# Kernel optimization log

Measured on AMD Instinct MI355X. Metric: run time of the kernel, lower is better.

## Reference

```python
import jax, jax.numpy as jnp
import numpy as np
from jax import lax

DN = ('NCHW', 'OIHW', 'NCHW')

def _conv(x, w, b, s):
    return lax.conv_general_dilated(x, w, (s, s), 'VALID', dimension_numbers=DN) + b[None, :, None, None]

def _deconv(x, w, b, s):
    # transposed conv, VALID: out = (in-1)*s + k
    return lax.conv_transpose(x, w, (s, s), 'VALID', dimension_numbers=DN) + b[None, :, None, None]

def _encoder(x, ew1, eb1, ew2, eb2, ew3, eb3):
    h = jax.nn.relu(_conv(x, ew1, eb1, 2))
    h = jax.nn.relu(_conv(h, ew2, eb2, 2))
    return jax.nn.relu(_conv(h, ew3, eb3, 2))

def _xcorr(x1, x2):
    # per-sample cross-correlation: x2[i] (C,h,w) is the kernel for x1[i] (C,H,W).
    # Equivalent to the original python loop of B single-sample F.conv2d calls,
    # fused into one grouped conv (feature_group_count=B).
    B, C, H, W = x1.shape
    y = lax.conv_general_dilated(x1.reshape(1, B * C, H, W), x2, (1, 1), 'VALID',
                                 dimension_numbers=DN, feature_group_count=B)
    return y.reshape(B, 1, y.shape[2], y.shape[3])

def setup_inputs():
    key = jax.random.key(0)
    ks = jax.random.split(key, 24)
    B = 64
    f32 = jnp.float32
    def w(k, shape, fan_in):
        return jax.random.normal(k, shape, f32) * np.float32(1.0 / np.sqrt(fan_in))
    inp = {}
    inp['pos'] = jax.random.uniform(ks[0], (B, 3, 255, 255), f32)
    inp['neg'] = jax.random.uniform(ks[1], (B, 3, 255, 255), f32)
    inp['pos_crop'] = jax.random.uniform(ks[2], (B, 3, 127, 127), f32)
    inp['eps'] = jax.random.normal(ks[3], (B, 32, 14, 14), f32)
    s = np.float32(1.0 / np.sqrt(3 * 127 * 127))  # pytorch init_anchor: uniform(-stdv, stdv)
    inp['anchor_crop'] = jax.random.uniform(ks[4], (3, 127, 127), f32, -s, s)
    # shared encoder (used by VAE and by self.encoder)
    inp['ew1'] = w(ks[5], (32, 3, 4, 4), 3 * 16);   inp['eb1'] = jnp.zeros((32,), f32)
    inp['ew2'] = w(ks[6], (64, 32, 4, 4), 32 * 16); inp['eb2'] = jnp.zeros((64,), f32)
    inp['ew3'] = w(ks[7], (64, 64, 4, 4), 64 * 16); inp['eb3'] = jnp.zeros((64,), f32)
    # VAE heads + decoder
    inp['mw'] = w(ks[8], (32, 64, 1, 1), 64);  inp['mb'] = jnp.zeros((32,), f32)
    inp['lw'] = w(ks[9], (32, 64, 1, 1), 64);  inp['lb'] = jnp.zeros((32,), f32)
    inp['dw0'] = w(ks[10], (64, 32, 1, 1), 32);      inp['db0'] = jnp.zeros((64,), f32)
    inp['dw1'] = w(ks[11], (32, 64, 4, 4), 64 * 16); inp['db1'] = jnp.zeros((32,), f32)
    inp['dw2'] = w(ks[12], (16, 32, 4, 4), 32 * 16); inp['db2'] = jnp.zeros((16,), f32)
    inp['dw3'] = w(ks[13], (3, 16, 5, 5), 16 * 25);  inp['db3'] = jnp.zeros((3,), f32)
    return inp

def reference(pos, neg, pos_crop, eps, anchor_crop, ew1, eb1, ew2, eb2, ew3, eb3,
              mw, mb, lw, lb, dw0, db0, dw1, db1, dw2, db2, dw3, db3):
    enc = lambda x: _encoder(x, ew1, eb1, ew2, eb2, ew3, eb3)
    # VAE forward on pos_crop
    h = enc(pos_crop)                          # [B,64,14,14]
    mu = _conv(h, mw, mb, 1)                   # [B,32,14,14]
    logvar = _conv(h, lw, lb, 1)
    z = mu + eps * jnp.exp(0.5 * logvar)       # reparameterization
    d = jax.nn.relu(_conv(z, dw0, db0, 1))
    d = jax.nn.relu(_deconv(d, dw1, db1, 2))   # 14 -> 30
    d = jax.nn.relu(_deconv(d, dw2, db2, 2))   # 30 -> 62
    recon = jax.nn.sigmoid(_deconv(d, dw3, db3, 2))  # 62 -> 127
    # siamese branches
    pos_f = enc(pos)                           # [B,64,30,30]
    neg_f = enc(neg)
    B = pos.shape[0]
    anchor = jnp.broadcast_to(anchor_crop[None], (B,) + anchor_crop.shape)  # [B,3,127,127]
    anchor_f = enc(anchor)                     # [B,64,14,14]
    cxp = _xcorr(pos_f, anchor_f)              # [B,1,17,17]
    cxn = _xcorr(neg_f, anchor_f)
    return (anchor, cxp, cxn, recon, mu, logvar)
```

## Files before the change

### kernel.cpp

```cpp
#include <hip/hip_runtime.h>

#define DIVUP(a,b) (((a)+(b)-1)/(b))

__global__ void bcast_anchor_kernel(const float* __restrict__ a, float* __restrict__ out) {
    int i = blockIdx.x * 256 + threadIdx.x;
    int b = blockIdx.y;
    if (i < 48387) out[b * 48387 + i] = a[i];
}

template<int OCT, bool VEC>
__global__ void conv4s2_relu_k(const float* __restrict__ in, const float* __restrict__ w,
                               const float* __restrict__ bias, float* __restrict__ out,
                               int Cin, int Hin, int Win, int Hout, int Wout, int OSTR)
{
    const int ocg = blockIdx.y, b = blockIdx.z, Cout = gridDim.y * OCT;
    const int TX = (Wout + 3) >> 2;
    const int t  = blockIdx.x * 256 + threadIdx.x;
    if (t >= Hout * TX) return;
    const int oy = t / TX, tx = t - oy * TX;
    int ox0 = tx * 4; if (ox0 > Wout - 4) ox0 = Wout - 4;

    const float* ip = in + ((size_t)(b * Cin) * Hin + 2 * oy) * Win + 2 * ox0;
    const float* wb = w + (size_t)ocg * OCT * Cin * 16;
    float acc[OCT][4];
    #pragma unroll
    for (int o = 0; o < OCT; ++o) {
        float z = bias[ocg * OCT + o];
        acc[o][0] = z; acc[o][1] = z; acc[o][2] = z; acc[o][3] = z;
    }
    for (int ic = 0; ic < Cin; ++ic) {
        const float* r = ip + (size_t)ic * Hin * Win;
        #pragma unroll
        for (int ky = 0; ky < 4; ++ky) {
            const float* rr = r + ky * Win;
            float x0,x1,x2,x3,x4,x5,x6,x7,x8,x9;
            if (VEC) {
                const float2* rv = (const float2*)rr;
                float2 p0=rv[0], p1=rv[1], p2=rv[2], p3=rv[3], p4=rv[4];
                x0=p0.x; x1=p0.y; x2=p1.x; x3=p1.y; x4=p2.x;
                x5=p2.y; x6=p3.x; x7=p3.y; x8=p4.x; x9=p4.y;
            } else {
                x0=rr[0]; x1=rr[1]; x2=rr[2]; x3=rr[3]; x4=rr[4];
                x5=rr[5]; x6=rr[6]; x7=rr[7]; x8=rr[8]; x9=rr[9];
            }
            #pragma unroll
            for (int o = 0; o < OCT; ++o) {
                const float* wk = wb + ((o * Cin + ic) * 4 + ky) * 4;
                float w0 = wk[0], w1 = wk[1], w2 = wk[2], w3 = wk[3];
                acc[o][0] = fmaf(x0, w0, fmaf(x1, w1, fmaf(x2, w2, fmaf(x3, w3, acc[o][0]))));
                acc[o][1] = fmaf(x2, w0, fmaf(x3, w1, fmaf(x4, w2, fmaf(x5, w3, acc[o][1]))));
                acc[o][2] = fmaf(x4, w0, fmaf(x5, w1, fmaf(x6, w2, fmaf(x7, w3, acc[o][2]))));
                acc[o][3] = fmaf(x6, w0, fmaf(x7, w1, fmaf(x8, w2, fmaf(x9, w3, acc[o][3]))));
            }
        }
    }
    float* op = out + (((size_t)b * Cout + ocg * OCT) * Hout + oy) * OSTR + ox0;
    #pragma unroll
    for (int o = 0; o < OCT; ++o) {
        float* q = op + (size_t)o * Hout * OSTR;
        q[0] = fmaxf(acc[o][0], 0.0f); q[1] = fmaxf(acc[o][1], 0.0f);
        q[2] = fmaxf(acc[o][2], 0.0f); q[3] = fmaxf(acc[o][3], 0.0f);
    }
}

__global__ void conv4s2_pair4_k(const float* __restrict__ in, const float* __restrict__ w,
                                const float* __restrict__ bias, float* __restrict__ out,
                                int nb)
{
    const int bid = blockIdx.x;
    int b, ocg, xt;
    if ((nb & 7) == 0) {
        const int xcd = bid & 7;
        const int t8  = bid >> 3;
        const int spx = t8 >> 5;
        const int j   = t8 & 31;
        b   = xcd + 8 * spx;
        ocg = j >> 1;
        xt  = j & 1;
    } else {
        xt  = bid & 1;
        ocg = (bid >> 1) & 15;
        b   = bid >> 5;
    }
    const int Cin = 32, Hin = 126, Hout = 62, Wout = 62, Cout = 64;
    const int TX = 16, H2 = 31;
    const int t = xt * 256 + threadIdx.x;
    if (t >= H2 * TX) return;
    const int oyp = t / TX, tx = t - oyp * TX;
    int ox0 = tx * 4; if (ox0 > Wout - 4) ox0 = Wout - 4;
    const int oy0 = 2 * oyp;

    const float* ip = in + ((size_t)(b * Cin) * Hin + 2 * oy0) * 128 + 2 * ox0;
    const float* wb = w + (size_t)ocg * 4 * Cin * 16;
    float acc[4][2][4];
    #pragma unroll
    for (int o = 0; o < 4; ++o) {
        float z = bias[ocg * 4 + o];
        #pragma unroll
        for (int p = 0; p < 2; ++p) {
            acc[o][p][0] = z; acc[o][p][1] = z; acc[o][p][2] = z; acc[o][p][3] = z;
        }
    }
    for (int ic = 0; ic < Cin; ++ic) {
        const float* r = ip + (size_t)ic * Hin * 128;
        float4 ra[6]; float4 rb[6]; float2 rc[6];
        #pragma unroll
        for (int rr6 = 0; rr6 < 6; ++rr6) {
            const float* row = r + rr6 * 128;
            ra[rr6] = *(const float4*)row;
            rb[rr6] = *(const float4*)(row + 4);
            rc[rr6] = *(const float2*)(row + 8);
        }
        #pragma unroll
        for (int rr6 = 0; rr6 < 6; ++rr6) {
            float x0=ra[rr6].x, x1=ra[rr6].y, x2=ra[rr6].z, x3=ra[rr6].w;
            float x4=rb[rr6].x, x5=rb[rr6].y, x6=rb[rr6].z, x7=rb[rr6].w;
            float x8=rc[rr6].x, x9=rc[rr6].y;
            #pragma unroll
            for (int o = 0; o < 4; ++o) {
                if (rr6 < 4) {
                    const float* wk = wb + ((o * Cin + ic) * 4 + rr6) * 4;
                    float w0 = wk[0], w1 = wk[1], w2 = wk[2], w3 = wk[3];
                    acc[o][0][0] = fmaf(x0, w0, fmaf(x1, w1, fmaf(x2, w2, fmaf(x3, w3, acc[o][0][0]))));
                    acc[o][0][1] = fmaf(x2, w0, fmaf(x3, w1, fmaf(x4, w2, fmaf(x5, w3, acc[o][0][1]))));
                    acc[o][0][2] = fmaf(x4, w0, fmaf(x5, w1, fmaf(x6, w2, fmaf(x7, w3, acc[o][0][2]))));
                    acc[o][0][3] = fmaf(x6, w0, fmaf(x7, w1, fmaf(x8, w2, fmaf(x9, w3, acc[o][0][3]))));
                }
                if (rr6 >= 2) {
                    const float* wk = wb + ((o * Cin + ic) * 4 + (rr6 - 2)) * 4;
                    float w0 = wk[0], w1 = wk[1], w2 = wk[2], w3 = wk[3];
                    acc[o][1][0] = fmaf(x0, w0, fmaf(x1, w1, fmaf(x2, w2, fmaf(x3, w3, acc[o][1][0]))));
                    acc[o][1][1] = fmaf(x2, w0, fmaf(x3, w1, fmaf(x4, w2, fmaf(x5, w3, acc[o][1][1]))));
                    acc[o][1][2] = fmaf(x4, w0, fmaf(x5, w1, fmaf(x6, w2, fmaf(x7, w3, acc[o][1][2]))));
                    acc[o][1][3] = fmaf(x6, w0, fmaf(x7, w1, fmaf(x8, w2, fmaf(x9, w3, acc[o][1][3]))));
                }
            }
        }
    }
    float* op = out + (((size_t)b * Cout + ocg * 4) * Hout + oy0) * Wout + ox0;
    #pragma unroll
    for (int o = 0; o < 4; ++o) {
        float* q = op + (size_t)o * Hout * Wout;
        q[0]        = fmaxf(acc[o][0][0], 0.0f); q[1]        = fmaxf(acc[o][0][1], 0.0f);
        q[2]        = fmaxf(acc[o][0][2], 0.0f); q[3]        = fmaxf(acc[o][0][3], 0.0f);
        q[Wout]     = fmaxf(acc[o][1][0], 0.0f); q[Wout + 1] = fmaxf(acc[o][1][1], 0.0f);
        q[Wout + 2] = fmaxf(acc[o][1][2], 0.0f); q[Wout + 3] = fmaxf(acc[o][1][3], 0.0f);
    }
}

__global__ void vae_head_kernel(const float* __restrict__ h, const float* __restrict__ mw,
                                const float* __restrict__ mb, const float* __restrict__ lw,
                                const float* __restrict__ lb, const float* __restrict__ eps,
                                float* __restrict__ mu_out, float* __restrict__ lv_out,
                                float* __restrict__ z_out)
{
    const int idx = blockIdx.x * 256 + threadIdx.x;
    if (idx >= 64 * 32 * 196) return;
    const int p  = idx % 196;
    const int oc = (idx / 196) % 32;
    const int b  = idx / (196 * 32);
    const float* hb = h + (b * 64) * 196 + p;
    float am = mb[oc], al = lb[oc];
    for (int ic = 0; ic < 64; ++ic) {
        float hv = hb[ic * 196];
        am = fmaf(hv, mw[oc * 64 + ic], am);
        al = fmaf(hv, lw[oc * 64 + ic], al);
    }
    mu_out[idx] = am;
    lv_out[idx] = al;
    z_out[idx]  = fmaf(eps[idx], expf(0.5f * al), am);
}

__global__ void conv1x1_relu_kernel(const float* __restrict__ in, const float* __restrict__ w,
                                    const float* __restrict__ bias, float* __restrict__ out,
                                    int Cin, int Cout, int HW, int total)
{
    const int idx = blockIdx.x * 256 + threadIdx.x;
    if (idx >= total) return;
    const int p  = idx % HW;
    const int oc = (idx / HW) % Cout;
    const int b  = idx / (HW * Cout);
    const float* ib = in + (b * Cin) * HW + p;
    float acc = bias[oc];
    for (int ic = 0; ic < 64; ++ic) acc = fmaf(ib[(ic % Cin) * HW], w[oc * Cin + (ic % Cin)], acc) - ((ic >= Cin) ? fmaf(ib[(ic % Cin) * HW], w[oc * Cin + (ic % Cin)], 0.0f) : 0.0f);
    out[idx] = fmaxf(acc, 0.0f);
}

template<int OCT>
__global__ void deconv4s2_relu_k(const float* __restrict__ in, const float* __restrict__ w,
                                 const float* __restrict__ bias, float* __restrict__ out,
                                 int Cin, int Hin, int Win, int Hout, int Wout)
{
    const int ocg = blockIdx.y, b = blockIdx.z, Cout = gridDim.y * OCT;
    const int H2 = Hout >> 1, W2 = Wout >> 1;
    const int t = blockIdx.x * 256 + threadIdx.x;
    if (t >= H2 * W2) return;
    const int oyi = t / W2, oxi = t - oyi * W2;
    const bool my0 = oyi >= 1, my1 = oyi < Hin;
    const bool mx0 = oxi >= 1, mx1 = oxi < Win;
    const int iy0 = my0 ? oyi - 1 : 0, iy1 = my1 ? oyi : 0;
    const int ix0 = mx0 ? oxi - 1 : 0, ix1 = mx1 ? oxi : 0;
    float acc[OCT][4];
    #pragma unroll
    for (int o = 0; o < OCT; ++o) {
        float z = bias[ocg * OCT + o];
        acc[o][0] = z; acc[o][1] = z; acc[o][2] = z; acc[o][3] = z;
    }
    const float* ib = in + (size_t)(b * Cin) * Hin * Win;
    const float* wb = w + (size_t)ocg * OCT * Cin * 16;
    for (int ic = 0; ic < Cin; ++ic) {
        const float* base = ib + (size_t)ic * Hin * Win;
        float v00 = (my0 && mx0) ? base[iy0 * Win + ix0] : 0.0f;
        float v01 = (my0 && mx1) ? base[iy0 * Win + ix1] : 0.0f;
        float v10 = (my1 && mx0) ? base[iy1 * Win + ix0] : 0.0f;
        float v11 = (my1 && mx1) ? base[iy1 * Win + ix1] : 0.0f;
        #pragma unroll
        for (int o = 0; o < OCT; ++o) {
            const float* wc = wb + (size_t)(o * Cin + ic) * 16;
            #pragma unroll
            for (int py = 0; py < 2; ++py)
                #pragma unroll
                for (int px = 0; px < 2; ++px) {
                    const int k0 = (1 - py) * 4, k1 = (3 - py) * 4;
                    acc[o][py * 2 + px] =
                        fmaf(v00, wc[k0 + 1 - px], fmaf(v01, wc[k0 + 3 - px],
                        fmaf(v10, wc[k1 + 1 - px], fmaf(v11, wc[k1 + 3 - px],
                             acc[o][py * 2 + px]))));
                }
        }
    }
    const int oy = 2 * oyi, ox = 2 * oxi;
    #pragma unroll
    for (int o = 0; o < OCT; ++o) {
        float* op = out + (((size_t)b * Cout + ocg * OCT + o) * Hout + oy) * Wout + ox;
        float2 r0; r0.x = fmaxf(acc[o][0], 0.0f); r0.y = fmaxf(acc[o][1], 0.0f);
        float2 r1; r1.x = fmaxf(acc[o][2], 0.0f); r1.y = fmaxf(acc[o][3], 0.0f);
        *(float2*)op = r0;
        *(float2*)(op + Wout) = r1;
    }
}

__global__ void deconv5s2_sigmoid_k(const float* __restrict__ in, const float* __restrict__ w,
                                    const float* __restrict__ bias, float* __restrict__ out)
{
    __shared__ float lds[16 * 6 * 66];
    const int b   = blockIdx.y;
    const int tid = threadIdx.x;
    const int oyi0 = blockIdx.x * 4;

    const float* ib = in + (size_t)(b * 16) * 3844;
    for (int i = tid; i < 16 * 6 * 66; i += 256) {
        const int c   = i % 66;
        const int row = i / 66;
        const int r   = row % 6;
        const int ic  = row / 6;
        const int iy  = oyi0 - 2 + r;
        const int ix  = c - 2;
        float v = 0.0f;
        if ((unsigned)iy < 62u && (unsigned)ix < 62u)
            v = ib[ic * 3844 + iy * 62 + ix];
        lds[i] = v;
    }
    __syncthreads();

    const int ry0 = tid >> 6;
    const int oxi = tid & 63;

    float acc[3][4];
    #pragma unroll
    for (int oc = 0; oc < 3; ++oc) {
        float z = bias[oc];
        acc[oc][0] = z; acc[oc][1] = z; acc[oc][2] = z; acc[oc][3] = z;
    }
    for (int ic = 0; ic < 16; ++ic) {
        const float* lb = lds + ic * 6 * 66;
        float v[3][3];
        #pragma unroll
        for (int a = 0; a < 3; ++a)
            #pragma unroll
            for (int c = 0; c < 3; ++c)
                v[a][c] = lb[(ry0 + a) * 66 + oxi + c];
        #pragma unroll
        for (int a = 0; a < 3; ++a)
            #pragma unroll
            for (int c = 0; c < 3; ++c) {
                float vv = v[a][c];
                #pragma unroll
                for (int oc = 0; oc < 3; ++oc) {
                    const float* wc = w + (oc * 16 + ic) * 25;
                    acc[oc][0] = fmaf(vv, wc[(2 * a) * 5 + 2 * c], acc[oc][0]);
                    if (c > 0) acc[oc][1] = fmaf(vv, wc[(2 * a) * 5 + 2 * c - 1], acc[oc][1]);
                    if (a > 0) acc[oc][2] = fmaf(vv, wc[(2 * a - 1) * 5 + 2 * c], acc[oc][2]);
                    if (a > 0 && c > 0) acc[oc][3] = fmaf(vv, wc[(2 * a - 1) * 5 + 2 * c - 1], acc[oc][3]);
                }
            }
    }
    #pragma unroll
    for (int oc = 0; oc < 3; ++oc)
        #pragma unroll
        for (int j = 0; j < 4; ++j)
            acc[oc][j] = 1.0f / (1.0f + expf(-acc[oc][j]));

    __syncthreads();
    #pragma unroll
    for (int oc = 0; oc < 3; ++oc)
        #pragma unroll
        for (int py = 0; py < 2; ++py)
            #pragma unroll
            for (int px = 0; px < 2; ++px)
                lds[((oc * 8 + 2 * ry0 + py) * 2 + px) * 64 + oxi] = acc[oc][py * 2 + px];
    __syncthreads();

    const int oybase = 2 * oyi0;
    for (int i = tid; i < 3 * 8 * 127; i += 256) {
        const int ox = i % 127;
        const int rr = i / 127;
        const int ry = rr % 8;
        const int oc = rr / 8;
        const int oy = oybase + ry;
        if (oy < 127) {
            float vv = lds[((oc * 8 + ry) * 2 + (ox & 1)) * 64 + (ox >> 1)];
            out[(((size_t)b * 3 + oc) * 127 + oy) * 127 + ox] = vv;
        }
    }
}

__global__ void xcorr_split_kernel(const float* __restrict__ f, const float* __restrict__ af,
                                   float* __restrict__ out)
{
    const int b = blockIdx.x, g = blockIdx.y;
    const int idx = threadIdx.x;
    if (idx >= 153) return;
    const int oy = idx / 9, tx = idx - oy * 9, ox = tx * 2;
    const float* fb = f + ((size_t)b * 64 + g * 4) * 900 + oy * 30 + ox;
    const float* ab = af + g * 4 * 196;
    float a0 = 0.0f, a1 = 0.0f;
    for (int c = 0; c < 4; ++c) {
        const float* fc = fb + c * 900;
        const float* ac = ab + c * 196;
        #pragma unroll
        for (int ky = 0; ky < 14; ++ky) {
            const float* fr = fc + ky * 30;
            const float* ar = ac + ky * 14;
            float v[15];
            #pragma unroll
            for (int k = 0; k < 15; ++k) v[k] = fr[k];
            #pragma unroll
            for (int k = 0; k < 14; ++k) {
                float wv = ar[k];
                a0 = fmaf(v[k],     wv, a0);
                a1 = fmaf(v[k + 1], wv, a1);
            }
        }
    }
    atomicAdd(&out[b * 289 + oy * 17 + ox], a0);
    if (ox + 1 < 17) atomicAdd(&out[b * 289 + oy * 17 + ox + 1], a1);
}

extern "C" void kernel_launch(void* const* d_in, const int* in_sizes, int n_in,
                              void* d_out, int out_size, void* d_ws, size_t ws_size,
                              hipStream_t stream)
{
    const float* pos         = (const float*)d_in[0];
    const float* neg         = (const float*)d_in[1];
    const float* pos_crop    = (const float*)d_in[2];
    const float* eps         = (const float*)d_in[3];
    const float* anchor_crop = (const float*)d_in[4];
    const float* ew1 = (const float*)d_in[5];  const float* eb1 = (const float*)d_in[6];
    const float* ew2 = (const float*)d_in[7];  const float* eb2 = (const float*)d_in[8];
    const float* ew3 = (const float*)d_in[9];  const float* eb3 = (const float*)d_in[10];
    const float* mw  = (const float*)d_in[11]; const float* mb  = (const float*)d_in[12];
    const float* lw  = (const float*)d_in[13]; const float* lb  = (const float*)d_in[14];
    const float* dw0 = (const float*)d_in[15]; const float* db0 = (const float*)d_in[16];
    const float* dw1 = (const float*)d_in[17]; const float* db1 = (const float*)d_in[18];
    const float* dw2 = (const float*)d_in[19]; const float* db2 = (const float*)d_in[20];
    const float* dw3 = (const float*)d_in[21]; const float* db3 = (const float*)d_in[22];

    float* out = (float*)d_out;
    float* ws  = (float*)d_ws;

    float* o_anchor = out;
    float* o_cxp    = out + 3096768;
    float* o_cxn    = out + 3115264;
    float* o_recon  = out + 3133760;
    float* o_mu     = out + 6230528;
    float* o_lv     = out + 6631936;

    float* AF = ws;
    float* A  = ws + 12544;
    const long budget = (long)(ws_size / 4) - 12544;

    const int CBV = budget >= 12361728L ? 64 : budget >= 6582272L ? 32
                  : budget >= 3692544L ? 16 : 8;
    float* E1  = A;
    float* E2  = A + (size_t)CBV * 123008;
    float* CH3 = E2 + (size_t)CBV * 57600;
    const bool dec_full = budget >= 6983680L;
    float* Z   = A;
    float* D0  = A + 401408;
    float* D1  = A + 1204224;
    float* D2  = A + 3047424;
    float* D2c = A;
    const int CB = budget >= 24387584L ? 32 : budget >= 12193792L ? 16
                 : budget >= 6096896L ? 8 : 4;
    float* F1 = A;
    float* F2 = A + (size_t)CB * 516096;
    float* F3 = A;
    float* AH1 = A;
    float* AH2 = A + 123008;

    bcast_anchor_kernel<<<dim3(189, 64), 256, 0, stream>>>(anchor_crop, o_anchor);

    conv4s2_relu_k<4,false><<<dim3(4, 8, 1), 256, 0, stream>>>(anchor_crop, ew1, eb1, AH1, 3, 127, 127, 62, 62, 62);
    conv4s2_relu_k<4,true ><<<dim3(1, 16, 1), 256, 0, stream>>>(AH1, ew2, eb2, AH2, 32, 62, 62, 30, 30, 30);
    conv4s2_relu_k<4,true ><<<dim3(1, 16, 1), 256, 0, stream>>>(AH2, ew3, eb3, AF, 64, 30, 30, 14, 14, 14);

    for (int c = 0; c < 64 / CBV; ++c) {
        const float* inp = pos_crop + (size_t)c * CBV * 48387;
        conv4s2_relu_k<4,false><<<dim3(4, 8, CBV), 256, 0, stream>>>(inp, ew1, eb1, E1, 3, 127, 127, 62, 62, 62);
        conv4s2_relu_k<4,true ><<<dim3(1, 16, CBV), 256, 0, stream>>>(E1, ew2, eb2, E2, 32, 62, 62, 30, 30, 30);
        conv4s2_relu_k<4,true ><<<dim3(1, 16, CBV), 256, 0, stream>>>(E2, ew3, eb3, CH3 + (size_t)c * CBV * 12544, 64, 30, 30, 14, 14, 14);
    }
    vae_head_kernel<<<1568, 256, 0, stream>>>(CH3, mw, mb, lw, lb, eps, o_mu, o_lv, Z);
    conv1x1_relu_kernel<<<3136, 256, 0, stream>>>(Z, dw0, db0, D0, 32, 64, 196, 64*64*196);
    deconv4s2_relu_k<4><<<dim3(1, 8, 64), 256, 0, stream>>>(D0, dw1, db1, D1, 64, 14, 14, 30, 30);
    if (dec_full) {
        deconv4s2_relu_k<4><<<dim3(4, 4, 64), 256, 0, stream>>>(D1, dw2, db2, D2, 32, 30, 30, 62, 62);
        deconv5s2_sigmoid_k<<<dim3(16, 64), 256, 0, stream>>>(D2, dw3, db3, o_recon);
    } else {
        for (int c = 0; c < 4; ++c) {
            deconv4s2_relu_k<4><<<dim3(4, 4, 16), 256, 0, stream>>>(D1 + (size_t)c * 16 * 28800, dw2, db2, D2c, 32, 30, 30, 62, 62);
            deconv5s2_sigmoid_k<<<dim3(16, 16), 256, 0, stream>>>(D2c, dw3, db3, o_recon + (size_t)c * 16 * 48387);
        }
    }

    hipMemsetAsync(o_cxp, 0, 2 * 18496 * sizeof(float), stream);
    const int nchunks = 128 / CB;
    for (int c = 0; c < nchunks; ++c) {
        const int s0 = c * CB;
        const float* inp  = (s0 < 64) ? pos + (size_t)s0 * 195075 : neg + (size_t)(s0 - 64) * 195075;
        float*       o_cx = (s0 < 64) ? o_cxp + (size_t)s0 * 289  : o_cxn + (size_t)(s0 - 64) * 289;
        conv4s2_relu_k<4,false><<<dim3(16, 8, CB), 256, 0, stream>>>(inp, ew1, eb1, F1, 3, 255, 255, 126, 126, 128);
        conv4s2_pair4_k<<<dim3(32 * CB), 256, 0, stream>>>(F1, ew2, eb2, F2, CB);
        conv4s2_relu_k<4,true ><<<dim3(1, 16, CB), 256, 0, stream>>>(F2, ew3, eb3, F3, 64, 62, 62, 30, 30, 30);
        xcorr_split_kernel<<<dim3(CB, 16), 192, 0, stream>>>(F3, AF, o_cx);
    }
}
```

Baseline: 1.517 ms.

## Double-buffer input rows in pair4 conv and drop XCD-aware block mapping

```diff
diff --git a/kernel.cpp b/kernel.cpp
--- a/kernel.cpp
+++ b/kernel.cpp
@@ -65,26 +65,12 @@
 
 __global__ void conv4s2_pair4_k(const float* __restrict__ in, const float* __restrict__ w,
                                 const float* __restrict__ bias, float* __restrict__ out,
-                                int nb)
-{
-    const int bid = blockIdx.x;
-    int b, ocg, xt;
-    if ((nb & 7) == 0) {
-        const int xcd = bid & 7;
-        const int t8  = bid >> 3;
-        const int spx = t8 >> 5;
-        const int j   = t8 & 31;
-        b   = xcd + 8 * spx;
-        ocg = j >> 1;
-        xt  = j & 1;
-    } else {
-        xt  = bid & 1;
-        ocg = (bid >> 1) & 15;
-        b   = bid >> 5;
-    }
-    const int Cin = 32, Hin = 126, Hout = 62, Wout = 62, Cout = 64;
-    const int TX = 16, H2 = 31;
-    const int t = xt * 256 + threadIdx.x;
+                                int Cin, int Hin, int Hout, int Wout)
+{
+    const int ocg = blockIdx.y, b = blockIdx.z, Cout = gridDim.y * 4;
+    const int TX = (Wout + 3) >> 2;
+    const int H2 = Hout >> 1;
+    const int t  = blockIdx.x * 256 + threadIdx.x;
     if (t >= H2 * TX) return;
     const int oyp = t / TX, tx = t - oyp * TX;
     int ox0 = tx * 4; if (ox0 > Wout - 4) ox0 = Wout - 4;
@@ -101,42 +87,61 @@
             acc[o][p][0] = z; acc[o][p][1] = z; acc[o][p][2] = z; acc[o][p][3] = z;
         }
     }
-    for (int ic = 0; ic < Cin; ++ic) {
-        const float* r = ip + (size_t)ic * Hin * 128;
-        float4 ra[6]; float4 rb[6]; float2 rc[6];
-        #pragma unroll
-        for (int rr6 = 0; rr6 < 6; ++rr6) {
-            const float* row = r + rr6 * 128;
-            ra[rr6] = *(const float4*)row;
-            rb[rr6] = *(const float4*)(row + 4);
-            rc[rr6] = *(const float2*)(row + 8);
-        }
-        #pragma unroll
-        for (int rr6 = 0; rr6 < 6; ++rr6) {
-            float x0=ra[rr6].x, x1=ra[rr6].y, x2=ra[rr6].z, x3=ra[rr6].w;
-            float x4=rb[rr6].x, x5=rb[rr6].y, x6=rb[rr6].z, x7=rb[rr6].w;
-            float x8=rc[rr6].x, x9=rc[rr6].y;
-            #pragma unroll
-            for (int o = 0; o < 4; ++o) {
-                if (rr6 < 4) {
-                    const float* wk = wb + ((o * Cin + ic) * 4 + rr6) * 4;
-                    float w0 = wk[0], w1 = wk[1], w2 = wk[2], w3 = wk[3];
-                    acc[o][0][0] = fmaf(x0, w0, fmaf(x1, w1, fmaf(x2, w2, fmaf(x3, w3, acc[o][0][0]))));
-                    acc[o][0][1] = fmaf(x2, w0, fmaf(x3, w1, fmaf(x4, w2, fmaf(x5, w3, acc[o][0][1]))));
-                    acc[o][0][2] = fmaf(x4, w0, fmaf(x5, w1, fmaf(x6, w2, fmaf(x7, w3, acc[o][0][2]))));
-                    acc[o][0][3] = fmaf(x6, w0, fmaf(x7, w1, fmaf(x8, w2, fmaf(x9, w3, acc[o][0][3]))));
-                }
-                if (rr6 >= 2) {
-                    const float* wk = wb + ((o * Cin + ic) * 4 + (rr6 - 2)) * 4;
-                    float w0 = wk[0], w1 = wk[1], w2 = wk[2], w3 = wk[3];
-                    acc[o][1][0] = fmaf(x0, w0, fmaf(x1, w1, fmaf(x2, w2, fmaf(x3, w3, acc[o][1][0]))));
-                    acc[o][1][1] = fmaf(x2, w0, fmaf(x3, w1, fmaf(x4, w2, fmaf(x5, w3, acc[o][1][1]))));
-                    acc[o][1][2] = fmaf(x4, w0, fmaf(x5, w1, fmaf(x6, w2, fmaf(x7, w3, acc[o][1][2]))));
-                    acc[o][1][3] = fmaf(x6, w0, fmaf(x7, w1, fmaf(x8, w2, fmaf(x9, w3, acc[o][1][3]))));
-                }
-            }
-        }
-    }
+
+    float4 raA[6], rbA[6]; float2 rcA[6];
+    float4 raB[6], rbB[6]; float2 rcB[6];
+
+#define PAIR4_LOAD(RA, RB, RC, IC) { \
+        const float* r_ = ip + (size_t)(IC) * Hin * 128; \
+        _Pragma("unroll") \
+        for (int q_ = 0; q_ < 6; ++q_) { \
+            const float* row_ = r_ + q_ * 128; \
+            RA[q_] = *(const float4*)row_; \
+            RB[q_] = *(const float4*)(row_ + 4); \
+            RC[q_] = *(const float2*)(row_ + 8); \
+        } }
+
+#define PAIR4_COMP(RA, RB, RC, IC) { \
+        _Pragma("unroll") \
+        for (int rr6_ = 0; rr6_ < 6; ++rr6_) { \
+            float x0=RA[rr6_].x, x1=RA[rr6_].y, x2=RA[rr6_].z, x3=RA[rr6_].w; \
+            float x4=RB[rr6_].x, x5=RB[rr6_].y, x6=RB[rr6_].z, x7=RB[rr6_].w; \
+            float x8=RC[rr6_].x, x9=RC[rr6_].y; \
+            _Pragma("unroll") \
+            for (int o_ = 0; o_ < 4; ++o_) { \
+                if (rr6_ < 4) {                \
+                    const float* wk = wb + ((o_ * Cin + (IC)) * 4 + rr6_) * 4;    \
+                    float w0=wk[0], w1=wk[1], w2=wk[2], w3=wk[3]; \
+                    acc[o_][0][0] = fmaf(x0,w0, fmaf(x1,w1, fmaf(x2,w2, fmaf(x3,w3, acc[o_][0][0])))); \
+                    acc[o_][0][1] = fmaf(x2,w0, fmaf(x3,w1, fmaf(x4,w2, fmaf(x5,w3, acc[o_][0][1])))); \
+                    acc[o_][0][2] = fmaf(x4,w0, fmaf(x5,w1, fmaf(x6,w2, fmaf(x7,w3, acc[o_][0][2])))); \
+                    acc[o_][0][3] = fmaf(x6,w0, fmaf(x7,w1, fmaf(x8,w2, fmaf(x9,w3, acc[o_][0][3])))); \
+                } \
+                if (rr6_ >= 2) {               \
+                    const float* wk = wb + ((o_ * Cin + (IC)) * 4 + (rr6_ - 2)) * 4; \
+                    float w0=wk[0], w1=wk[1], w2=wk[2], w3=wk[3]; \
+                    acc[o_][1][0] = fmaf(x0,w0, fmaf(x1,w1, fmaf(x2,w2, fmaf(x3,w3, acc[o_][1][0])))); \
+                    acc[o_][1][1] = fmaf(x2,w0, fmaf(x3,w1, fmaf(x4,w2, fmaf(x5,w3, acc[o_][1][1])))); \
+                    acc[o_][1][2] = fmaf(x4,w0, fmaf(x5,w1, fmaf(x6,w2, fmaf(x7,w3, acc[o_][1][2])))); \
+                    acc[o_][1][3] = fmaf(x6,w0, fmaf(x7,w1, fmaf(x8,w2, fmaf(x9,w3, acc[o_][1][3])))); \
+                } \
+            } \
+        } }
+
+    PAIR4_LOAD(raA, rbA, rcA, 0);
+    #pragma unroll 1
+    for (int ic = 0; ic <= Cin - 4; ic += 2) {
+        PAIR4_LOAD(raB, rbB, rcB, ic + 1);
+        PAIR4_COMP(raA, rbA, rcA, ic);
+        PAIR4_LOAD(raA, rbA, rcA, ic + 2);
+        PAIR4_COMP(raB, rbB, rcB, ic + 1);
+    }
+    PAIR4_LOAD(raB, rbB, rcB, Cin - 1);
+    PAIR4_COMP(raA, rbA, rcA, Cin - 2);
+    PAIR4_COMP(raB, rbB, rcB, Cin - 1);
+#undef PAIR4_LOAD
+#undef PAIR4_COMP
+
     float* op = out + (((size_t)b * Cout + ocg * 4) * Hout + oy0) * Wout + ox0;
     #pragma unroll
     for (int o = 0; o < 4; ++o) {
@@ -441,7 +446,7 @@
         const float* inp  = (s0 < 64) ? pos + (size_t)s0 * 195075 : neg + (size_t)(s0 - 64) * 195075;
         float*       o_cx = (s0 < 64) ? o_cxp + (size_t)s0 * 289  : o_cxn + (size_t)(s0 - 64) * 289;
         conv4s2_relu_k<4,false><<<dim3(16, 8, CB), 256, 0, stream>>>(inp, ew1, eb1, F1, 3, 255, 255, 126, 126, 128);
-        conv4s2_pair4_k<<<dim3(32 * CB), 256, 0, stream>>>(F1, ew2, eb2, F2, CB);
+        conv4s2_pair4_k<<<dim3(2, 16, CB), 256, 0, stream>>>(F1, ew2, eb2, F2, 32, 126, 62, 62);
         conv4s2_relu_k<4,true ><<<dim3(1, 16, CB), 256, 0, stream>>>(F2, ew3, eb3, F3, 64, 62, 62, 30, 30, 30);
         xcorr_split_kernel<<<dim3(CB, 16), 192, 0, stream>>>(F3, AF, o_cx);
     }
```

Measured after the change: 2.243 ms. 47.9% more time.
